# Performance work log

Hardware: AMD Instinct MI355X
Metric: run time of the kernel (lower is better)

## Reference

```python
import jax, jax.numpy as jnp
import numpy as np

B, L, IN_LEN = 1, 1024, 512
D_MODEL, N_LAYERS = 1024, 4
D_INNER = 2 * D_MODEL
D_STATE = 16
DT_RANK = D_MODEL // 16  # 64
D_CONV = 4
EPS = 1e-5


def setup_inputs() -> dict:
    key = jax.random.key(0)
    ks = jax.random.split(key, 12)
    s = 0.02
    # dt bias init as in mamba_ssm: softplus^{-1}(dt) with dt ~ logUniform(1e-3, 1e-1)
    dt = jnp.exp(jax.random.uniform(ks[7], (N_LAYERS, D_INNER)) * (jnp.log(0.1) - jnp.log(0.001)) + jnp.log(0.001))
    dt_bias = dt + jnp.log(-jnp.expm1(-dt))
    A_log = jnp.log(jnp.broadcast_to(jnp.arange(1, D_STATE + 1, dtype=jnp.float32), (N_LAYERS, D_INNER, D_STATE)))
    return {
        "input": jax.random.normal(ks[0], (B, L, IN_LEN), jnp.float32),
        "inference_parameters": 0,
        "input_w": jax.random.normal(ks[1], (D_MODEL, IN_LEN), jnp.float32) * s,
        "norm_w": jnp.ones((N_LAYERS, D_MODEL), jnp.float32),
        "norm_b": jnp.zeros((N_LAYERS, D_MODEL), jnp.float32),
        "in_proj_w": jax.random.normal(ks[2], (N_LAYERS, 2 * D_INNER, D_MODEL), jnp.float32) * s,
        "conv_w": jax.random.normal(ks[3], (N_LAYERS, D_INNER, D_CONV), jnp.float32) * 0.3,
        "conv_b": jnp.zeros((N_LAYERS, D_INNER), jnp.float32),
        "x_proj_w": jax.random.normal(ks[4], (N_LAYERS, DT_RANK + 2 * D_STATE, D_INNER), jnp.float32) * s,
        "dt_proj_w": jax.random.normal(ks[5], (N_LAYERS, D_INNER, DT_RANK), jnp.float32) * (DT_RANK ** -0.5),
        "dt_proj_b": dt_bias,
        "A_log": A_log,
        "ssm_D": jnp.ones((N_LAYERS, D_INNER), jnp.float32),
        "out_proj_w": jax.random.normal(ks[6], (N_LAYERS, D_MODEL, D_INNER), jnp.float32) * s,
    }


def _layer_norm(x, w, b):
    mu = x.mean(-1, keepdims=True)
    xc = x - mu
    var = (xc * xc).mean(-1, keepdims=True)
    return xc * jax.lax.rsqrt(var + EPS) * w + b


def _mamba(h, ipw, cw, cb, xpw, dtw, dtb, a_log, d_skip, opw):
    # h: [B, L, D_MODEL]
    seqlen = h.shape[1]
    xz = jnp.einsum('bld,ed->ble', h, ipw)  # [B, L, 2*D_INNER]
    x, z = jnp.split(xz, 2, axis=-1)
    # causal depthwise conv1d (kernel D_CONV, left pad D_CONV-1)
    xp = jnp.pad(x, ((0, 0), (D_CONV - 1, 0), (0, 0)))
    x = sum(cw[:, k] * xp[:, k:k + seqlen, :] for k in range(D_CONV)) + cb
    x = jax.nn.silu(x)
    x_dbl = jnp.einsum('bld,ed->ble', x, xpw)  # [B, L, DT_RANK + 2*D_STATE]
    dt = x_dbl[..., :DT_RANK]
    Bc = x_dbl[..., DT_RANK:DT_RANK + D_STATE]  # [B, L, D_STATE]
    Cc = x_dbl[..., DT_RANK + D_STATE:]          # [B, L, D_STATE]
    delta = jax.nn.softplus(jnp.einsum('blr,dr->bld', dt, dtw) + dtb)  # [B, L, D_INNER]
    A = -jnp.exp(a_log)                          # [D_INNER, D_STATE]
    dA = jnp.exp(delta[..., None] * A)           # [B, L, D_INNER, D_STATE]
    dBu = delta[..., None] * Bc[:, :, None, :] * x[..., None]

    def step(hc, t):
        dA_t, dBu_t, C_t = t
        hc = dA_t * hc + dBu_t                   # [B, D_INNER, D_STATE]
        return hc, jnp.einsum('bds,bs->bd', hc, C_t)

    h0 = jnp.zeros((x.shape[0], D_INNER, D_STATE), x.dtype)
    _, ys = jax.lax.scan(step, h0, (dA.transpose(1, 0, 2, 3), dBu.transpose(1, 0, 2, 3), Cc.transpose(1, 0, 2)))
    y = ys.transpose(1, 0, 2) + x * d_skip       # [B, L, D_INNER]
    y = y * jax.nn.silu(z)
    return jnp.einsum('bld,ed->ble', y, opw)     # [B, L, D_MODEL]


def reference(input, inference_parameters, input_w, norm_w, norm_b, in_proj_w, conv_w, conv_b, x_proj_w, dt_proj_w, dt_proj_b, A_log, ssm_D, out_proj_w):
    h = jnp.einsum('bli,di->bld', input, input_w)  # input_layer (no bias)
    res = None
    for i in range(N_LAYERS):
        res = h if res is None else h + res
        hn = _layer_norm(res, norm_w[i], norm_b[i])
        h = _mamba(hn, in_proj_w[i], conv_w[i], conv_b[i], x_proj_w[i], dt_proj_w[i], dt_proj_b[i], A_log[i], ssm_D[i], out_proj_w[i])
    # NOTE: the source forward returns hidden_states directly (norm_f is never applied)
    return h
```

## Files before the change

kernel.cpp:

```cpp
#include <hip/hip_runtime.h>
#include <hip/hip_bf16.h>
#include <math.h>

#define L_SEQ   1024
#define DMODEL  1024
#define DINNER  2048
#define DSTATE  16
#define DTRANK  64
#define NXP     96
#define LN_EPS  1e-5f
#define CHUNK   16
#define NCHUNK  (L_SEQ / CHUNK)
#define SK(l)   ((l) + ((l) >> 5))

typedef __bf16 bf16x8 __attribute__((ext_vector_type(8)));
typedef float  f32x4  __attribute__((ext_vector_type(4)));

__global__ __launch_bounds__(256)
void gemm_bt_bf16(const __hip_bfloat16* __restrict__ A,
                  const __hip_bfloat16* __restrict__ W,
                  float* __restrict__ C,
                  int K, int lda, int ldb, int ldc) {
    __shared__ __hip_bfloat16 As[128][32];
    __shared__ __hip_bfloat16 Bs[128][32];
    const int tid  = threadIdx.x;
    const int lane = tid & 63;
    const int wave = tid >> 6;
    const int m0 = blockIdx.y * 128, n0 = blockIdx.x * 128;
    const int wm = (wave >> 1) * 64, wn = (wave & 1) * 64;
    const int srow = tid >> 2, skcol = (tid & 3) << 3;
    const int fm = lane & 15, fk = (lane >> 4) << 3;

    f32x4 acc[4][4] = {};

    const __hip_bfloat16* Ap0 = A + (size_t)(m0 + srow) * lda + skcol;
    const __hip_bfloat16* Ap1 = Ap0 + (size_t)64 * lda;
    const __hip_bfloat16* Wp0 = W + (size_t)(n0 + srow) * ldb + skcol;
    const __hip_bfloat16* Wp1 = Wp0 + (size_t)64 * ldb;

    for (int k0 = 0; k0 < K; k0 += 32) {
        __syncthreads();
        __builtin_amdgcn_global_load_lds(
            (const __attribute__((address_space(1))) unsigned int*)(Ap0 + k0),
            (__attribute__((address_space(3))) unsigned int*)&As[srow][skcol], 16, 0, 0);
        __builtin_amdgcn_global_load_lds(
            (const __attribute__((address_space(1))) unsigned int*)(Ap1 + k0),
            (__attribute__((address_space(3))) unsigned int*)&As[64 + srow][skcol], 16, 0, 0);
        __builtin_amdgcn_global_load_lds(
            (const __attribute__((address_space(1))) unsigned int*)(Wp0 + k0),
            (__attribute__((address_space(3))) unsigned int*)&Bs[srow][skcol], 16, 0, 0);
        __builtin_amdgcn_global_load_lds(
            (const __attribute__((address_space(1))) unsigned int*)(Wp1 + k0),
            (__attribute__((address_space(3))) unsigned int*)&Bs[64 + srow][skcol], 16, 0, 0);
        __syncthreads();

        bf16x8 af[4], bfr[4];
        #pragma unroll
        for (int i = 0; i < 4; ++i) {
            af[i]  = *(const bf16x8*)&As[wm + i * 16 + fm][fk];
            bfr[i] = *(const bf16x8*)&Bs[wn + i * 16 + fm][fk];
        }
        #pragma unroll
        for (int mt = 0; mt < 4; ++mt)
            #pragma unroll
            for (int nt = 0; nt < 4; ++nt)
                acc[mt][nt] = __builtin_amdgcn_mfma_f32_16x16x32_bf16(
                    af[mt], bfr[nt], acc[mt][nt], 0, 0, 0);
    }

    const int crow = (lane >> 4) << 2;
    const int ccol = lane & 15;
    #pragma unroll
    for (int mt = 0; mt < 4; ++mt)
        #pragma unroll
        for (int nt = 0; nt < 4; ++nt) {
            float* cp = C + (size_t)(m0 + wm + mt * 16 + crow) * ldc
                          + n0 + wn + nt * 16 + ccol;
            #pragma unroll
            for (int r = 0; r < 4; ++r) cp[(size_t)r * ldc] = acc[mt][nt][r];
        }
}

__global__ __launch_bounds__(256)
void gemm_bt_bf16_sk(const __hip_bfloat16* __restrict__ A,
                     const __hip_bfloat16* __restrict__ W,
                     float* __restrict__ C,
                     int kchunk, int lda, int ldb, int ldc) {
    __shared__ __hip_bfloat16 As[128][32];
    __shared__ __hip_bfloat16 Bs[128][32];
    const int tid  = threadIdx.x;
    const int lane = tid & 63;
    const int wave = tid >> 6;
    const int m0 = blockIdx.y * 128, n0 = blockIdx.x * 128;
    const int k0s = blockIdx.z * kchunk;
    const int wm = (wave >> 1) * 64, wn = (wave & 1) * 64;
    const int srow = tid >> 2, skcol = (tid & 3) << 3;
    const int fm = lane & 15, fk = (lane >> 4) << 3;

    f32x4 acc[4][4] = {};

    const __hip_bfloat16* Ap0 = A + (size_t)(m0 + srow) * lda + skcol;
    const __hip_bfloat16* Ap1 = Ap0 + (size_t)64 * lda;
    const __hip_bfloat16* Wp0 = W + (size_t)(n0 + srow) * ldb + skcol;
    const __hip_bfloat16* Wp1 = Wp0 + (size_t)64 * ldb;

    for (int k0 = k0s; k0 < k0s + kchunk; k0 += 32) {
        __syncthreads();
        __builtin_amdgcn_global_load_lds(
            (const __attribute__((address_space(1))) unsigned int*)(Ap0 + k0),
            (__attribute__((address_space(3))) unsigned int*)&As[srow][skcol], 16, 0, 0);
        __builtin_amdgcn_global_load_lds(
            (const __attribute__((address_space(1))) unsigned int*)(Ap1 + k0),
            (__attribute__((address_space(3))) unsigned int*)&As[64 + srow][skcol], 16, 0, 0);
        __builtin_amdgcn_global_load_lds(
            (const __attribute__((address_space(1))) unsigned int*)(Wp0 + k0),
            (__attribute__((address_space(3))) unsigned int*)&Bs[srow][skcol], 16, 0, 0);
        __builtin_amdgcn_global_load_lds(
            (const __attribute__((address_space(1))) unsigned int*)(Wp1 + k0),
            (__attribute__((address_space(3))) unsigned int*)&Bs[64 + srow][skcol], 16, 0, 0);
        __syncthreads();

        bf16x8 af[4], bfr[4];
        #pragma unroll
        for (int i = 0; i < 4; ++i) {
            af[i]  = *(const bf16x8*)&As[wm + i * 16 + fm][fk];
            bfr[i] = *(const bf16x8*)&Bs[wn + i * 16 + fm][fk];
        }
        #pragma unroll
        for (int mt = 0; mt < 4; ++mt)
            #pragma unroll
            for (int nt = 0; nt < 4; ++nt)
                acc[mt][nt] = __builtin_amdgcn_mfma_f32_16x16x32_bf16(
                    af[mt], bfr[nt], acc[mt][nt], 0, 0, 0);
    }

    const int crow = (lane >> 4) << 2;
    const int ccol = lane & 15;
    #pragma unroll
    for (int mt = 0; mt < 4; ++mt)
        #pragma unroll
        for (int nt = 0; nt < 4; ++nt) {
            float* cp = C + (size_t)(m0 + wm + mt * 16 + crow) * ldc
                          + n0 + wn + nt * 16 + ccol;
            #pragma unroll
            for (int r = 0; r < 4; ++r)
                atomicAdd(&cp[(size_t)r * ldc], acc[mt][nt][r]);
        }
}

__global__ __launch_bounds__(256)
void gemm_nt(const float* __restrict__ A, const float* __restrict__ W,
             float* __restrict__ C, int M, int N, int K,
             int lda, int ldb, int ldc) {
    __shared__ float As[16][64];
    __shared__ float Bs[16][64];
    const int tid = threadIdx.x;
    const int tx = tid & 15, ty = tid >> 4;
    const int m0 = blockIdx.y * 64, n0 = blockIdx.x * 64;
    const int lr = tid >> 2;
    const int lk = (tid & 3) << 2;
    float acc[4][4] = {};

    for (int k0 = 0; k0 < K; k0 += 16) {
        float4 av = make_float4(0.f, 0.f, 0.f, 0.f);
        float4 bv = make_float4(0.f, 0.f, 0.f, 0.f);
        const int am = m0 + lr;
        if (am < M) av = *(const float4*)(A + (size_t)am * lda + k0 + lk);
        const int bn = n0 + lr;
        if (bn < N) bv = *(const float4*)(W + (size_t)bn * ldb + k0 + lk);
        __syncthreads();
        As[lk + 0][lr] = av.x; As[lk + 1][lr] = av.y;
        As[lk + 2][lr] = av.z; As[lk + 3][lr] = av.w;
        Bs[lk + 0][lr] = bv.x; Bs[lk + 1][lr] = bv.y;
        Bs[lk + 2][lr] = bv.z; Bs[lk + 3][lr] = bv.w;
        __syncthreads();
        #pragma unroll
        for (int k = 0; k < 16; ++k) {
            const float4 a = *(const float4*)&As[k][ty << 2];
            const float4 b = *(const float4*)&Bs[k][tx << 2];
            acc[0][0] += a.x * b.x; acc[0][1] += a.x * b.y;
            acc[0][2] += a.x * b.z; acc[0][3] += a.x * b.w;
            acc[1][0] += a.y * b.x; acc[1][1] += a.y * b.y;
            acc[1][2] += a.y * b.z; acc[1][3] += a.y * b.w;
            acc[2][0] += a.z * b.x; acc[2][1] += a.z * b.y;
            acc[2][2] += a.z * b.z; acc[2][3] += a.z * b.w;
            acc[3][0] += a.w * b.x; acc[3][1] += a.w * b.y;
            acc[3][2] += a.w * b.z; acc[3][3] += a.w * b.w;
        }
    }
    #pragma unroll
    for (int i = 0; i < 4; ++i) {
        const int m = m0 + (ty << 2) + i;
        if (m < M) {
            #pragma unroll
            for (int j = 0; j < 4; ++j) {
                const int n = n0 + (tx << 2) + j;
                if (n < N) C[(size_t)m * ldc + n] = acc[i][j];
            }
        }
    }
}

__global__ __launch_bounds__(256)
void gemm_nn_softplus(const float* __restrict__ A, const float* __restrict__ B,
                      const float* __restrict__ bias, float* __restrict__ C,
                      int K, int lda, int ldb, int ldc) {
    __shared__ float As[16][64];
    __shared__ float Bs[16][64];
    const int t = threadIdx.x;
    const int tx = t & 15, ty = t >> 4;
    const int m0 = blockIdx.y * 64, n0 = blockIdx.x * 64;
    const int ar = t >> 2, ak = (t & 3) << 2;
    const int bk = t >> 4, bn = (t & 15) << 2;
    float acc[4][4] = {};

    for (int k0 = 0; k0 < K; k0 += 16) {
        const float4 av = *(const float4*)(A + (size_t)(m0 + ar) * lda + k0 + ak);
        const float4 bv = *(const float4*)(B + (size_t)(k0 + bk) * ldb + n0 + bn);
        __syncthreads();
        As[ak + 0][ar] = av.x; As[ak + 1][ar] = av.y;
        As[ak + 2][ar] = av.z; As[ak + 3][ar] = av.w;
        *(float4*)&Bs[bk][bn] = bv;
        __syncthreads();
        #pragma unroll
        for (int k = 0; k < 16; ++k) {
            const float4 a = *(const float4*)&As[k][ty << 2];
            const float4 b = *(const float4*)&Bs[k][tx << 2];
            acc[0][0] += a.x * b.x; acc[0][1] += a.x * b.y;
            acc[0][2] += a.x * b.z; acc[0][3] += a.x * b.w;
            acc[1][0] += a.y * b.x; acc[1][1] += a.y * b.y;
            acc[1][2] += a.y * b.z; acc[1][3] += a.y * b.w;
            acc[2][0] += a.z * b.x; acc[2][1] += a.z * b.y;
            acc[2][2] += a.z * b.z; acc[2][3] += a.z * b.w;
            acc[3][0] += a.w * b.x; acc[3][1] += a.w * b.y;
            acc[3][2] += a.w * b.z; acc[3][3] += a.w * b.w;
        }
    }
    #pragma unroll
    for (int i = 0; i < 4; ++i) {
        const int m = m0 + (ty << 2) + i;
        const float bb = bias[m];
        #pragma unroll
        for (int j = 0; j < 4; ++j) {
            const int n = n0 + (tx << 2) + j;
            const float v = acc[i][j] + bb;
            C[(size_t)m * ldc + n] = (v > 20.f) ? v : log1pf(expf(v));
        }
    }
}

__global__ __launch_bounds__(256)
void gemm_nn_splitk(const float* __restrict__ A, const float* __restrict__ B,
                    float* __restrict__ C, int lda, int ldb, int ldc, int kchunk) {
    __shared__ float As[32][32];
    __shared__ float Bs[32][64];
    const int t = threadIdx.x;
    const int tx = t & 15, ty = t >> 4;
    const int m0 = blockIdx.y * 32, n0 = blockIdx.x * 64;
    const int k0s = blockIdx.z * kchunk;
    const int ar = t >> 3, ak = (t & 7) << 2;
    const int bk = t >> 4, bn = (t & 15) << 2;
    float acc[2][4] = {};

    for (int k0 = k0s; k0 < k0s + kchunk; k0 += 32) {
        const float4 av = *(const float4*)(A + (size_t)(m0 + ar) * lda + k0 + ak);
        const float4 bv0 = *(const float4*)(B + (size_t)(k0 + bk) * ldb + n0 + bn);
        const float4 bv1 = *(const float4*)(B + (size_t)(k0 + bk + 16) * ldb + n0 + bn);
        __syncthreads();
        As[ak + 0][ar] = av.x; As[ak + 1][ar] = av.y;
        As[ak + 2][ar] = av.z; As[ak + 3][ar] = av.w;
        *(float4*)&Bs[bk][bn] = bv0;
        *(float4*)&Bs[bk + 16][bn] = bv1;
        __syncthreads();
        #pragma unroll
        for (int k = 0; k < 32; ++k) {
            const float a0 = As[k][(ty << 1) + 0];
            const float a1 = As[k][(ty << 1) + 1];
            const float4 b = *(const float4*)&Bs[k][tx << 2];
            acc[0][0] += a0 * b.x; acc[0][1] += a0 * b.y;
            acc[0][2] += a0 * b.z; acc[0][3] += a0 * b.w;
            acc[1][0] += a1 * b.x; acc[1][1] += a1 * b.y;
            acc[1][2] += a1 * b.z; acc[1][3] += a1 * b.w;
        }
    }
    #pragma unroll
    for (int i = 0; i < 2; ++i) {
        const int m = m0 + (ty << 1) + i;
        #pragma unroll
        for (int j = 0; j < 4; ++j)
            atomicAdd(&C[(size_t)m * ldc + n0 + (tx << 2) + j], acc[i][j]);
    }
}

__global__ __launch_bounds__(256)
void zero_f32(float* __restrict__ p, int n) {
    const int i = blockIdx.x * 256 + threadIdx.x;
    if (i < n) p[i] = 0.f;
}

__global__ __launch_bounds__(256)
void cast_f32_bf16(const float* __restrict__ in, __hip_bfloat16* __restrict__ out,
                   int n4) {
    const int i = blockIdx.x * 256 + threadIdx.x;
    if (i < n4) {
        const float4 v = *(const float4*)(in + (size_t)i * 4);
        __hip_bfloat16 h0 = __float2bfloat16(v.x), h1 = __float2bfloat16(v.y);
        __hip_bfloat16 h2 = __float2bfloat16(v.z), h3 = __float2bfloat16(v.w);
        ushort4 p;
        p.x = *(unsigned short*)&h0; p.y = *(unsigned short*)&h1;
        p.z = *(unsigned short*)&h2; p.w = *(unsigned short*)&h3;
        *(ushort4*)((unsigned short*)out + (size_t)i * 4) = p;
    }
}

__global__ __launch_bounds__(256)
void transpose_bc(const float* __restrict__ xdbl_T, float* __restrict__ xbc) {
    __shared__ float tile[32][33];
    const int t = threadIdx.x;
    const int l0 = blockIdx.x * 32;
    const int s = t >> 3, lc = (t & 7) << 2;
    const float4 v = *(const float4*)(xdbl_T + (size_t)(DTRANK + s) * L_SEQ + l0 + lc);
    tile[s][lc + 0] = v.x; tile[s][lc + 1] = v.y;
    tile[s][lc + 2] = v.z; tile[s][lc + 3] = v.w;
    __syncthreads();
    const int l = t >> 3, sc = (t & 7) << 2;
    float4 w;
    w.x = tile[sc + 0][l]; w.y = tile[sc + 1][l];
    w.z = tile[sc + 2][l]; w.w = tile[sc + 3][l];
    *(float4*)(xbc + (size_t)(l0 + l) * 32 + sc) = w;
}

__global__ __launch_bounds__(256)
void transpose_bf16(const unsigned short* __restrict__ in,
                    unsigned short* __restrict__ out, int R, int Cc) {
    __shared__ unsigned short tile[64][65];
    const int t = threadIdx.x;
    const int r0 = blockIdx.y * 64, c0 = blockIdx.x * 64;
    const int tr = t >> 3, tc8 = (t & 7) << 3;
    #pragma unroll
    for (int i = 0; i < 2; ++i) {
        const int r = tr + i * 32;
        const ushort4 v0 = *(const ushort4*)(in + (size_t)(r0 + r) * Cc + c0 + tc8);
        const ushort4 v1 = *(const ushort4*)(in + (size_t)(r0 + r) * Cc + c0 + tc8 + 4);
        tile[r][tc8 + 0] = v0.x; tile[r][tc8 + 1] = v0.y;
        tile[r][tc8 + 2] = v0.z; tile[r][tc8 + 3] = v0.w;
        tile[r][tc8 + 4] = v1.x; tile[r][tc8 + 5] = v1.y;
        tile[r][tc8 + 6] = v1.z; tile[r][tc8 + 7] = v1.w;
    }
    __syncthreads();
    #pragma unroll
    for (int i = 0; i < 2; ++i) {
        const int r = tr + i * 32;
        ushort4 w0, w1;
        w0.x = tile[tc8 + 0][r]; w0.y = tile[tc8 + 1][r];
        w0.z = tile[tc8 + 2][r]; w0.w = tile[tc8 + 3][r];
        w1.x = tile[tc8 + 4][r]; w1.y = tile[tc8 + 5][r];
        w1.z = tile[tc8 + 6][r]; w1.w = tile[tc8 + 7][r];
        *(ushort4*)(out + (size_t)(c0 + r) * R + r0 + tc8)     = w0;
        *(ushort4*)(out + (size_t)(c0 + r) * R + r0 + tc8 + 4) = w1;
    }
}

__global__ __launch_bounds__(256)
void add_ln(const float* __restrict__ h, float* __restrict__ res,
            __hip_bfloat16* __restrict__ hn, const float* __restrict__ w,
            const float* __restrict__ b, int is_first) {
    const int l = blockIdx.x;
    const int t = threadIdx.x;
    float v[4];
    float s = 0.f, ss = 0.f;
    #pragma unroll
    for (int j = 0; j < 4; ++j) {
        const int d = t + j * 256;
        float x = h[(size_t)l * DMODEL + d];
        if (!is_first) x += res[(size_t)l * DMODEL + d];
        res[(size_t)l * DMODEL + d] = x;
        v[j] = x; s += x; ss += x * x;
    }
    #pragma unroll
    for (int o = 32; o > 0; o >>= 1) {
        s  += __shfl_down(s, o);
        ss += __shfl_down(ss, o);
    }
    __shared__ float sm[4], sm2[4];
    const int wid = t >> 6;
    if ((t & 63) == 0) { sm[wid] = s; sm2[wid] = ss; }
    __syncthreads();
    s  = sm[0] + sm[1] + sm[2] + sm[3];
    ss = sm2[0] + sm2[1] + sm2[2] + sm2[3];
    const float mu  = s * (1.f / DMODEL);
    const float var = ss * (1.f / DMODEL) - mu * mu;
    const float r   = rsqrtf(var + LN_EPS);
    #pragma unroll
    for (int j = 0; j < 4; ++j) {
        const int d = t + j * 256;
        hn[(size_t)l * DMODEL + d] = __float2bfloat16((v[j] - mu) * r * w[d] + b[d]);
    }
}

__global__ __launch_bounds__(256)
void conv_silu_t(const float* __restrict__ xz_T, float* __restrict__ xc_T,
                 const float* __restrict__ cw, const float* __restrict__ cb) {
    const int d = blockIdx.x;
    const int t = threadIdx.x;
    __shared__ float row[L_SEQ];
    *(float4*)&row[t << 2] = *(const float4*)(xz_T + (size_t)d * L_SEQ + (t << 2));
    __syncthreads();
    const float w0 = cw[d * 4 + 0], w1 = cw[d * 4 + 1];
    const float w2 = cw[d * 4 + 2], w3 = cw[d * 4 + 3];
    const float bb = cb[d];
    float o[4];
    #pragma unroll
    for (int j = 0; j < 4; ++j) {
        const int l = (t << 2) + j;
        float acc = bb + w3 * row[l];
        if (l >= 1) acc += w2 * row[l - 1];
        if (l >= 2) acc += w1 * row[l - 2];
        if (l >= 3) acc += w0 * row[l - 3];
        const float sig = 1.f / (1.f + __expf(-acc));
        o[j] = acc * sig;
    }
    *(float4*)(xc_T + (size_t)d * L_SEQ + (t << 2)) = make_float4(o[0], o[1], o[2], o[3]);
}

__global__ __launch_bounds__(1024)
void ssm_scan_t2(const float* __restrict__ delta_T,
                 const float* __restrict__ xc_T,
                 const float* __restrict__ xbc,
                 const float* __restrict__ xz_T,
                 const float* __restrict__ alog,
                 const float* __restrict__ dsk,
                 __hip_bfloat16* __restrict__ y_T) {
    const int d = blockIdx.x;
    const int t = threadIdx.x;
    const int s = t & 15;
    const int c = t >> 4;

    __shared__ float sdl[L_SEQ + 32], sxl[L_SEQ + 32];
    __shared__ float sz[L_SEQ], sy[L_SEQ];
    __shared__ float saprod[NCHUNK][DSTATE];
    __shared__ float shloc[NCHUNK][DSTATE];
    __shared__ float shstart[NCHUNK][DSTATE];

    if (t < 256) {
        const float4 v = ((const float4*)(delta_T + (size_t)d * L_SEQ))[t];
        const int l = t << 2;
        sdl[SK(l)] = v.x; sdl[SK(l + 1)] = v.y;
        sdl[SK(l + 2)] = v.z; sdl[SK(l + 3)] = v.w;
    } else if (t < 512) {
        const int tt = t - 256;
        const float4 v = ((const float4*)(xc_T + (size_t)d * L_SEQ))[tt];
        const int l = tt << 2;
        sxl[SK(l)] = v.x; sxl[SK(l + 1)] = v.y;
        sxl[SK(l + 2)] = v.z; sxl[SK(l + 3)] = v.w;
    } else if (t < 768) {
        ((float4*)sz)[t - 512] =
            ((const float4*)(xz_T + (size_t)(DINNER + d) * L_SEQ))[t - 512];
    }
    __syncthreads();

    const float A  = -expf(alog[d * DSTATE + s]);
    const int   l0 = c * CHUNK;

    float ap[CHUNK], hl[CHUNK];
    float aprod = 1.f, h = 0.f;
    #pragma unroll
    for (int j = 0; j < CHUNK; ++j) {
        const int l = l0 + j;
        const float dl = sdl[SK(l)];
        const float da = __expf(dl * A);
        h = da * h + dl * xbc[(size_t)l * 32 + s] * sxl[SK(l)];
        aprod *= da;
        ap[j] = aprod; hl[j] = h;
    }
    saprod[c][s] = aprod;
    shloc[c][s]  = h;
    __syncthreads();

    if (t < 16) {
        float hs = 0.f;
        for (int cc = 0; cc < NCHUNK; ++cc) {
            shstart[cc][t] = hs;
            hs = saprod[cc][t] * hs + shloc[cc][t];
        }
    }
    __syncthreads();

    const float h0 = shstart[c][s];
    const float Dk = dsk[d];
    #pragma unroll
    for (int j = 0; j < CHUNK; ++j) {
        const int l = l0 + j;
        const float hj = h0 * ap[j] + hl[j];
        float cch = hj * xbc[(size_t)l * 32 + 16 + s];
        cch += __shfl_xor(cch, 1, 16);
        cch += __shfl_xor(cch, 2, 16);
        cch += __shfl_xor(cch, 4, 16);
        cch += __shfl_xor(cch, 8, 16);
        if (s == 0) {
            const float xl  = sxl[SK(l)];
            const float zl  = sz[l];
            const float sig = 1.f / (1.f + __expf(-zl));
            sy[l] = (cch + xl * Dk) * (zl * sig);
        }
    }
    __syncthreads();

    if (t < 256) {
        const float4 v = ((const float4*)sy)[t];
        __hip_bfloat16 h0b = __float2bfloat16(v.x), h1b = __float2bfloat16(v.y);
        __hip_bfloat16 h2b = __float2bfloat16(v.z), h3b = __float2bfloat16(v.w);
        ushort4 p;
        p.x = *(unsigned short*)&h0b; p.y = *(unsigned short*)&h1b;
        p.z = *(unsigned short*)&h2b; p.w = *(unsigned short*)&h3b;
        *(ushort4*)((unsigned short*)y_T + (size_t)d * L_SEQ + (t << 2)) = p;
    }
}

extern "C" void kernel_launch(void* const* d_in, const int* in_sizes, int n_in,
                              void* d_out, int out_size, void* d_ws, size_t ws_size,
                              hipStream_t stream) {
    const float* input   = (const float*)d_in[0];
    const float* input_w = (const float*)d_in[2];
    const float* norm_w  = (const float*)d_in[3];
    const float* norm_b  = (const float*)d_in[4];
    const float* ipw     = (const float*)d_in[5];
    const float* cw      = (const float*)d_in[6];
    const float* cb      = (const float*)d_in[7];
    const float* xpw     = (const float*)d_in[8];
    const float* dtw     = (const float*)d_in[9];
    const float* dtb     = (const float*)d_in[10];
    const float* alog    = (const float*)d_in[11];
    const float* dsk     = (const float*)d_in[12];
    const float* opw     = (const float*)d_in[13];
    float* out = (float*)d_out;

    float* ws      = (float*)d_ws;
    float* h       = ws;
    float* res     = h       + (1u << 20);
    float* xz_T    = res     + (1u << 20);
    float* xc_T    = xz_T    + (4u << 20);
    float* xdbl_T  = xc_T    + (2u << 20);
    float* xbc     = xdbl_T  + (NXP * L_SEQ);
    float* delta_T = xbc     + (L_SEQ * 32);
    __hip_bfloat16* hn_bf  = (__hip_bfloat16*)(delta_T + (2u << 20));
    __hip_bfloat16* yT_bf  = hn_bf  + (1u << 20);
    __hip_bfloat16* y_bf   = yT_bf  + (2u << 20);
    __hip_bfloat16* ipw_bf = y_bf   + (2u << 20);
    __hip_bfloat16* opw_bf = ipw_bf + (4u << 20);

    const dim3 blk(256);

    gemm_nt<<<dim3(DMODEL / 64, L_SEQ / 64), blk, 0, stream>>>(
        input, input_w, h, L_SEQ, DMODEL, 512, 512, 512, DMODEL);

    for (int i = 0; i < 4; ++i) {
        cast_f32_bf16<<<(2 * DINNER * DMODEL / 4 + 255) / 256, blk, 0, stream>>>(
            ipw + (size_t)i * 2 * DINNER * DMODEL, ipw_bf, 2 * DINNER * DMODEL / 4);

        add_ln<<<L_SEQ, 256, 0, stream>>>(
            h, res, hn_bf, norm_w + i * DMODEL, norm_b + i * DMODEL, i == 0);

        gemm_bt_bf16<<<dim3(L_SEQ / 128, 2 * DINNER / 128), blk, 0, stream>>>(
            ipw_bf, hn_bf, xz_T, DMODEL, DMODEL, DMODEL, L_SEQ);

        conv_silu_t<<<DINNER, 256, 0, stream>>>(
            xz_T, xc_T, cw + i * DINNER * 4, cb + i * DINNER);

        zero_f32<<<(NXP * L_SEQ + 255) / 256, blk, 0, stream>>>(xdbl_T, NXP * L_SEQ);
        gemm_nn_splitk<<<dim3(L_SEQ / 64, 3, 8), blk, 0, stream>>>(
            xpw + (size_t)i * NXP * DINNER, xc_T, xdbl_T,
            DINNER, L_SEQ, L_SEQ, DINNER / 8);

        transpose_bc<<<L_SEQ / 32, 256, 0, stream>>>(xdbl_T, xbc);

        gemm_nn_softplus<<<dim3(L_SEQ / 64, DINNER / 64), blk, 0, stream>>>(
            dtw + (size_t)i * DINNER * DTRANK, xdbl_T, dtb + i * DINNER, delta_T,
            DTRANK, DTRANK, L_SEQ, L_SEQ);

        ssm_scan_t2<<<DINNER, 1024, 0, stream>>>(
            delta_T, xc_T, xbc, xz_T,
            alog + i * DINNER * DSTATE, dsk + i * DINNER, yT_bf);

        transpose_bf16<<<dim3(L_SEQ / 64, DINNER / 64), blk, 0, stream>>>(
            (const unsigned short*)yT_bf, (unsigned short*)y_bf, DINNER, L_SEQ);

        cast_f32_bf16<<<(DMODEL * DINNER / 4 + 255) / 256, blk, 0, stream>>>(
            opw + (size_t)i * DMODEL * DINNER, opw_bf, DMODEL * DINNER / 4);
        float* dst = (i == 3) ? out : h;
        zero_f32<<<(L_SEQ * DMODEL + 255) / 256, blk, 0, stream>>>(dst, L_SEQ * DMODEL);
        gemm_bt_bf16_sk<<<dim3(DMODEL / 128, L_SEQ / 128, 4), blk, 0, stream>>>(
            y_bf, opw_bf, dst, DINNER / 4, DINNER, DINNER, DMODEL);
    }
}
```

Before: 913.2 us.

## Halve SSM scan block size with recompute and merge cast/zero launches

The SSM scan now runs with 512 threads per block and 32-step chunks. It no longer keeps per-step prefix arrays in registers; the second pass recomputes the local recurrence from the propagated chunk start state. The two weight-cast kernels are merged into one launch, and the two zero-fill kernels into one, which is moved earlier in the layer. This cuts register pressure and the length of the serial inter-chunk pass, and removes launch overhead. The cost is recomputing the exps in the scan, plus a longer per-thread serial chain.

Result: faster. 829.4 us (-9.2%).

```diff
diff --git a/kernel.cpp b/kernel.cpp
--- a/kernel.cpp
+++ b/kernel.cpp
@@ -9,7 +9,7 @@
 #define DTRANK  64
 #define NXP     96
 #define LN_EPS  1e-5f
-#define CHUNK   16
+#define CHUNK   32
 #define NCHUNK  (L_SEQ / CHUNK)
 #define SK(l)   ((l) + ((l) >> 5))
 
@@ -293,24 +293,29 @@
 }
 
 __global__ __launch_bounds__(256)
-void zero_f32(float* __restrict__ p, int n) {
+void zero2(float* __restrict__ a, int na, float* __restrict__ b, int nb) {
     const int i = blockIdx.x * 256 + threadIdx.x;
-    if (i < n) p[i] = 0.f;
-}
-
-__global__ __launch_bounds__(256)
-void cast_f32_bf16(const float* __restrict__ in, __hip_bfloat16* __restrict__ out,
-                   int n4) {
-    const int i = blockIdx.x * 256 + threadIdx.x;
-    if (i < n4) {
-        const float4 v = *(const float4*)(in + (size_t)i * 4);
-        __hip_bfloat16 h0 = __float2bfloat16(v.x), h1 = __float2bfloat16(v.y);
-        __hip_bfloat16 h2 = __float2bfloat16(v.z), h3 = __float2bfloat16(v.w);
-        ushort4 p;
-        p.x = *(unsigned short*)&h0; p.y = *(unsigned short*)&h1;
-        p.z = *(unsigned short*)&h2; p.w = *(unsigned short*)&h3;
-        *(ushort4*)((unsigned short*)out + (size_t)i * 4) = p;
-    }
+    if (i < na) a[i] = 0.f;
+    else if (i < na + nb) b[i - na] = 0.f;
+}
+
+__global__ __launch_bounds__(256)
+void cast_weights(const float* __restrict__ ina, __hip_bfloat16* __restrict__ outa,
+                  int n4a, const float* __restrict__ inb,
+                  __hip_bfloat16* __restrict__ outb, int n4b) {
+    int i = blockIdx.x * 256 + threadIdx.x;
+    const float* in;
+    __hip_bfloat16* out;
+    if (i < n4a) { in = ina; out = outa; }
+    else if (i < n4a + n4b) { in = inb; out = outb; i -= n4a; }
+    else return;
+    const float4 v = *(const float4*)(in + (size_t)i * 4);
+    __hip_bfloat16 h0 = __float2bfloat16(v.x), h1 = __float2bfloat16(v.y);
+    __hip_bfloat16 h2 = __float2bfloat16(v.z), h3 = __float2bfloat16(v.w);
+    ushort4 p;
+    p.x = *(unsigned short*)&h0; p.y = *(unsigned short*)&h1;
+    p.z = *(unsigned short*)&h2; p.w = *(unsigned short*)&h3;
+    *(ushort4*)((unsigned short*)out + (size_t)i * 4) = p;
 }
 
 __global__ __launch_bounds__(256)
@@ -423,14 +428,14 @@
     *(float4*)(xc_T + (size_t)d * L_SEQ + (t << 2)) = make_float4(o[0], o[1], o[2], o[3]);
 }
 
-__global__ __launch_bounds__(1024)
-void ssm_scan_t2(const float* __restrict__ delta_T,
-                 const float* __restrict__ xc_T,
-                 const float* __restrict__ xbc,
-                 const float* __restrict__ xz_T,
-                 const float* __restrict__ alog,
-                 const float* __restrict__ dsk,
-                 __hip_bfloat16* __restrict__ y_T) {
+__global__ __launch_bounds__(512)
+void ssm_scan_t(const float* __restrict__ delta_T,
+                const float* __restrict__ xc_T,
+                const float* __restrict__ xbc,
+                const float* __restrict__ xz_T,
+                const float* __restrict__ alog,
+                const float* __restrict__ dsk,
+                __hip_bfloat16* __restrict__ y_T) {
     const int d = blockIdx.x;
     const int t = threadIdx.x;
     const int s = t & 15;
@@ -447,58 +452,55 @@
         const int l = t << 2;
         sdl[SK(l)] = v.x; sdl[SK(l + 1)] = v.y;
         sdl[SK(l + 2)] = v.z; sdl[SK(l + 3)] = v.w;
-    } else if (t < 512) {
+        ((float4*)sz)[t] = ((const float4*)(xz_T + (size_t)(DINNER + d) * L_SEQ))[t];
+    } else {
         const int tt = t - 256;
         const float4 v = ((const float4*)(xc_T + (size_t)d * L_SEQ))[tt];
         const int l = tt << 2;
         sxl[SK(l)] = v.x; sxl[SK(l + 1)] = v.y;
         sxl[SK(l + 2)] = v.z; sxl[SK(l + 3)] = v.w;
-    } else if (t < 768) {
-        ((float4*)sz)[t - 512] =
-            ((const float4*)(xz_T + (size_t)(DINNER + d) * L_SEQ))[t - 512];
     }
     __syncthreads();
 
     const float A  = -expf(alog[d * DSTATE + s]);
     const int   l0 = c * CHUNK;
 
-    float ap[CHUNK], hl[CHUNK];
     float aprod = 1.f, h = 0.f;
-    #pragma unroll
+    #pragma unroll 4
     for (int j = 0; j < CHUNK; ++j) {
         const int l = l0 + j;
         const float dl = sdl[SK(l)];
         const float da = __expf(dl * A);
         h = da * h + dl * xbc[(size_t)l * 32 + s] * sxl[SK(l)];
         aprod *= da;
-        ap[j] = aprod; hl[j] = h;
     }
     saprod[c][s] = aprod;
     shloc[c][s]  = h;
     __syncthreads();
 
-    if (t < 16) {
+    if (c == 0) {
         float hs = 0.f;
         for (int cc = 0; cc < NCHUNK; ++cc) {
-            shstart[cc][t] = hs;
-            hs = saprod[cc][t] * hs + shloc[cc][t];
-        }
-    }
-    __syncthreads();
-
-    const float h0 = shstart[c][s];
+            shstart[cc][s] = hs;
+            hs = saprod[cc][s] * hs + shloc[cc][s];
+        }
+    }
+    __syncthreads();
+
+    h = shstart[c][s];
     const float Dk = dsk[d];
-    #pragma unroll
+    #pragma unroll 4
     for (int j = 0; j < CHUNK; ++j) {
         const int l = l0 + j;
-        const float hj = h0 * ap[j] + hl[j];
-        float cch = hj * xbc[(size_t)l * 32 + 16 + s];
+        const float dl = sdl[SK(l)];
+        const float xl = sxl[SK(l)];
+        h = __expf(dl * A) * h + dl * xbc[(size_t)l * 32 + s] * xl;
+        float cch = h * xbc[(size_t)l * 32 + 16 + s];
         cch += __shfl_xor(cch, 1, 16);
         cch += __shfl_xor(cch, 2, 16);
         cch += __shfl_xor(cch, 4, 16);
         cch += __shfl_xor(cch, 8, 16);
         if (s == 0) {
-            const float xl  = sxl[SK(l)];
             const float zl  = sz[l];
             const float sig = 1.f / (1.f + __expf(-zl));
             sy[l] = (cch + xl * Dk) * (zl * sig);
@@ -508,11 +510,11 @@
 
     if (t < 256) {
         const float4 v = ((const float4*)sy)[t];
-        __hip_bfloat16 h0b = __float2bfloat16(v.x), h1b = __float2bfloat16(v.y);
-        __hip_bfloat16 h2b = __float2bfloat16(v.z), h3b = __float2bfloat16(v.w);
+        __hip_bfloat16 h0 = __float2bfloat16(v.x), h1 = __float2bfloat16(v.y);
+        __hip_bfloat16 h2 = __float2bfloat16(v.z), h3 = __float2bfloat16(v.w);
         ushort4 p;
-        p.x = *(unsigned short*)&h0b; p.y = *(unsigned short*)&h1b;
-        p.z = *(unsigned short*)&h2b; p.w = *(unsigned short*)&h3b;
+        p.x = *(unsigned short*)&h0; p.y = *(unsigned short*)&h1;
+        p.z = *(unsigned short*)&h2; p.w = *(unsigned short*)&h3;
         *(ushort4*)((unsigned short*)y_T + (size_t)d * L_SEQ + (t << 2)) = p;
     }
 }
@@ -550,24 +552,30 @@
     __hip_bfloat16* opw_bf = ipw_bf + (4u << 20);
 
     const dim3 blk(256);
+    const int n4_ipw = 2 * DINNER * DMODEL / 4;
+    const int n4_opw = DMODEL * DINNER / 4;
 
     gemm_nt<<<dim3(DMODEL / 64, L_SEQ / 64), blk, 0, stream>>>(
         input, input_w, h, L_SEQ, DMODEL, 512, 512, 512, DMODEL);
 
     for (int i = 0; i < 4; ++i) {
-        cast_f32_bf16<<<(2 * DINNER * DMODEL / 4 + 255) / 256, blk, 0, stream>>>(
-            ipw + (size_t)i * 2 * DINNER * DMODEL, ipw_bf, 2 * DINNER * DMODEL / 4);
+        cast_weights<<<(n4_ipw + n4_opw + 255) / 256, blk, 0, stream>>>(
+            ipw + (size_t)i * 2 * DINNER * DMODEL, ipw_bf, n4_ipw,
+            opw + (size_t)i * DMODEL * DINNER, opw_bf, n4_opw);
 
         add_ln<<<L_SEQ, 256, 0, stream>>>(
             h, res, hn_bf, norm_w + i * DMODEL, norm_b + i * DMODEL, i == 0);
 
+        float* dst = (i == 3) ? out : h;
+        zero2<<<(NXP * L_SEQ + L_SEQ * DMODEL + 255) / 256, blk, 0, stream>>>(
+            xdbl_T, NXP * L_SEQ, dst, L_SEQ * DMODEL);
+
         gemm_bt_bf16<<<dim3(L_SEQ / 128, 2 * DINNER / 128), blk, 0, stream>>>(
             ipw_bf, hn_bf, xz_T, DMODEL, DMODEL, DMODEL, L_SEQ);
 
         conv_silu_t<<<DINNER, 256, 0, stream>>>(
             xz_T, xc_T, cw + i * DINNER * 4, cb + i * DINNER);
 
-        zero_f32<<<(NXP * L_SEQ + 255) / 256, blk, 0, stream>>>(xdbl_T, NXP * L_SEQ);
         gemm_nn_splitk<<<dim3(L_SEQ / 64, 3, 8), blk, 0, stream>>>(
             xpw + (size_t)i * NXP * DINNER, xc_T, xdbl_T,
             DINNER, L_SEQ, L_SEQ, DINNER / 8);
@@ -578,17 +586,13 @@
             dtw + (size_t)i * DINNER * DTRANK, xdbl_T, dtb + i * DINNER, delta_T,
             DTRANK, DTRANK, L_SEQ, L_SEQ);
 
-        ssm_scan_t2<<<DINNER, 1024, 0, stream>>>(
+        ssm_scan_t<<<DINNER, 512, 0, stream>>>(
             delta_T, xc_T, xbc, xz_T,
             alog + i * DINNER * DSTATE, dsk + i * DINNER, yT_bf);
 
         transpose_bf16<<<dim3(L_SEQ / 64, DINNER / 64), blk, 0, stream>>>(
             (const unsigned short*)yT_bf, (unsigned short*)y_bf, DINNER, L_SEQ);
 
-        cast_f32_bf16<<<(DMODEL * DINNER / 4 + 255) / 256, blk, 0, stream>>>(
-            opw + (size_t)i * DMODEL * DINNER, opw_bf, DMODEL * DINNER / 4);
-        float* dst = (i == 3) ? out : h;
-        zero_f32<<<(L_SEQ * DMODEL + 255) / 256, blk, 0, stream>>>(dst, L_SEQ * DMODEL);
         gemm_bt_bf16_sk<<<dim3(DMODEL / 128, L_SEQ / 128, 4), blk, 0, stream>>>(
             y_bf, opw_bf, dst, DINNER / 4, DINNER, DINNER, DMODEL);
     }
```
